# Optimization experiments

Measured on AMD Instinct MI355X. Metric: run time of the kernel, lower is better.

## Reference

```python
import jax, jax.numpy as jnp
import numpy as np

DIM = 2048
KV_DIM = 1024
NUM_HEADS = 16
HEAD_DIM = DIM // NUM_HEADS  # 128
EPS = 1e-6
B, LQ, LKV = 2, 4096, 1024


def _rope_cos_sin(L, d, base=10000.0):
    inv_freq = 1.0 / (base ** (np.arange(0, d, 2, dtype=np.float32) / d))  # [d/2]
    freqs = np.arange(L, dtype=np.float32)[:, None] * inv_freq[None, :]   # [L, d/2]
    emb = np.concatenate([freqs, freqs], axis=-1)                          # [L, d]
    return jnp.asarray(np.cos(emb)), jnp.asarray(np.sin(emb))


def setup_inputs() -> dict:
    key = jax.random.key(0)
    ks = jax.random.split(key, 10)
    x = jax.random.normal(ks[0], (B, LQ, DIM), dtype=jnp.float32)
    y = jax.random.normal(ks[1], (B, LKV, KV_DIM), dtype=jnp.float32)
    xc, xs = _rope_cos_sin(LQ, HEAD_DIM)
    yc, ys = _rope_cos_sin(LKV, HEAD_DIM)
    x_cos = jnp.broadcast_to(xc[None], (B, LQ, HEAD_DIM))
    x_sin = jnp.broadcast_to(xs[None], (B, LQ, HEAD_DIM))
    y_cos = jnp.broadcast_to(yc[None], (B, LKV, HEAD_DIM))
    y_sin = jnp.broadcast_to(ys[None], (B, LKV, HEAD_DIM))
    s = 0.02
    Wq = jax.random.normal(ks[2], (DIM, DIM), dtype=jnp.float32) * s
    Wk = jax.random.normal(ks[3], (DIM, KV_DIM), dtype=jnp.float32) * s
    Wv = jax.random.normal(ks[4], (DIM, KV_DIM), dtype=jnp.float32) * s
    Wo = jax.random.normal(ks[5], (DIM, DIM), dtype=jnp.float32) * s
    bq = jnp.zeros((DIM,), jnp.float32)
    bk = jnp.zeros((DIM,), jnp.float32)
    bv = jnp.zeros((DIM,), jnp.float32)
    bo = jnp.zeros((DIM,), jnp.float32)
    rmsq_w = jnp.ones((DIM,), jnp.float32)
    rmsk_w = jnp.ones((DIM,), jnp.float32)
    ln_w = jnp.ones((KV_DIM,), jnp.float32)
    ln_b = jnp.zeros((KV_DIM,), jnp.float32)
    return dict(x=x, y=y, x_cos=x_cos, x_sin=x_sin, y_cos=y_cos, y_sin=y_sin,
                Wq=Wq, bq=bq, Wk=Wk, bk=bk, Wv=Wv, bv=bv, Wo=Wo, bo=bo,
                rmsq_w=rmsq_w, rmsk_w=rmsk_w, ln_w=ln_w, ln_b=ln_b)


def _rms_norm(t, w, eps=EPS):
    return t * jax.lax.rsqrt(jnp.mean(t * t, axis=-1, keepdims=True) + eps) * w


def _layer_norm(t, w, b, eps=EPS):
    mu = jnp.mean(t, axis=-1, keepdims=True)
    var = jnp.mean(jnp.square(t - mu), axis=-1, keepdims=True)
    return (t - mu) * jax.lax.rsqrt(var + eps) * w + b


def _rotate_half(t):
    d2 = t.shape[-1] // 2
    return jnp.concatenate([-t[..., d2:], t[..., :d2]], axis=-1)


def _apply_rope(t, cos, sin):
    # t: [B, L, H, D]; cos/sin: [B, L, D] -> unsqueeze head dim (unsqueeze_dim=2)
    cos = cos[:, :, None, :]
    sin = sin[:, :, None, :]
    return t * cos + _rotate_half(t) * sin


def _block_forward(x, y, x_cos, x_sin, y_cos, y_sin,
                   Wq, bq, Wk, bk, Wv, bv, Wo, bo,
                   rmsq_w, rmsk_w, ln_w, ln_b):
    Bb, Lq, D = x.shape
    Lk = y.shape[1]
    H, Dh = NUM_HEADS, HEAD_DIM
    # y pre-norm (block-level LayerNorm)
    yn = _layer_norm(y, ln_w, ln_b)
    # projections + RMSNorm on q/k
    q = _rms_norm(x @ Wq.T + bq, rmsq_w)   # [B, Lq, D]
    k = _rms_norm(yn @ Wk.T + bk, rmsk_w)  # [B, Lk, D]
    v = yn @ Wv.T + bv                     # [B, Lk, D]
    # split heads and apply RoPE
    q = _apply_rope(q.reshape(Bb, Lq, H, Dh), x_cos, x_sin)
    k = _apply_rope(k.reshape(Bb, Lk, H, Dh), y_cos, y_sin)
    v = v.reshape(Bb, Lk, H, Dh)
    # non-causal cross attention, scale = 1/sqrt(head_dim)
    scale = 1.0 / jnp.sqrt(jnp.asarray(Dh, q.dtype))
    scores = jnp.einsum('blhd,bmhd->bhlm', q, k) * scale
    probs = jax.nn.softmax(scores, axis=-1)
    out = jnp.einsum('bhlm,bmhd->blhd', probs, v).reshape(Bb, Lq, D)
    return out @ Wo.T + bo


def reference(x, y, x_cos, x_sin, y_cos, y_sin,
              Wq, bq, Wk, bk, Wv, bv, Wo, bo,
              rmsq_w, rmsk_w, ln_w, ln_b):
    return _block_forward(x, y, x_cos, x_sin, y_cos, y_sin,
                          Wq, bq, Wk, bk, Wv, bv, Wo, bo,
                          rmsq_w, rmsk_w, ln_w, ln_b)
```

## Files before the change

### kernel.cpp

```cpp
#include <hip/hip_runtime.h>


typedef __attribute__((ext_vector_type(8))) short    short8;
typedef __attribute__((ext_vector_type(8))) unsigned short ushort8;
typedef __attribute__((ext_vector_type(4))) unsigned short ushort4v;
typedef __attribute__((ext_vector_type(4))) float    f32x4;
typedef __attribute__((ext_vector_type(16))) float   f32x16;
typedef __attribute__((ext_vector_type(4))) unsigned int uint4v;

#define DEV __device__ __forceinline__

DEV unsigned short f2bf(float f) {
  unsigned int u = __builtin_bit_cast(unsigned int, f);
  u += 0x7FFFu + ((u >> 16) & 1u);
  return (unsigned short)(u >> 16);
}
DEV float bf2f(unsigned short h) {
  return __builtin_bit_cast(float, ((unsigned int)h) << 16);
}
DEV unsigned int cvtpk_bf16(float lo, float hi) {
  unsigned int r;
  asm("v_cvt_pk_bf16_f32 %0, %1, %2" : "=v"(r) : "v"(lo), "v"(hi));
  return r;
}
DEV short8 mk8(unsigned a, unsigned b, unsigned c, unsigned d) {
  uint4v t; t.x = a; t.y = b; t.z = c; t.w = d;
  return __builtin_bit_cast(short8, t);
}

DEV void gload_lds16(const void* g, void* l) {
  __builtin_amdgcn_global_load_lds(
      (const __attribute__((address_space(1))) void*)g,
      (__attribute__((address_space(3))) void*)l, 16, 0, 0);
}

__global__ __launch_bounds__(256) void prep_kernel(const float* __restrict__ y,
                                                   const float* __restrict__ lnw,
                                                   const float* __restrict__ lnb,
                                                   unsigned short* __restrict__ yn,
                                                   const float* __restrict__ x,
                                                   const float* __restrict__ Wq,
                                                   const float* __restrict__ Wk,
                                                   const float* __restrict__ Wv,
                                                   const float* __restrict__ Wo,
                                                   unsigned short* __restrict__ xb,
                                                   unsigned short* __restrict__ Wqb,
                                                   unsigned short* __restrict__ Wkb,
                                                   unsigned short* __restrict__ Wvb,
                                                   unsigned short* __restrict__ Wob) {
  const int t = threadIdx.x;
  if (blockIdx.x < 2048) {
    const int row = blockIdx.x;
    const float* yr = y + (size_t)row * 1024;
    float4 v = *(const float4*)(yr + t * 4);
    float s1 = v.x + v.y + v.z + v.w;
    float s2 = v.x * v.x + v.y * v.y + v.z * v.z + v.w * v.w;
#pragma unroll
    for (int m = 1; m < 64; m <<= 1) {
      s1 += __shfl_xor(s1, m);
      s2 += __shfl_xor(s2, m);
    }
    __shared__ float red[8];
    const int wave = t >> 6, lane = t & 63;
    if (lane == 0) { red[wave] = s1; red[4 + wave] = s2; }
    __syncthreads();
    s1 = red[0] + red[1] + red[2] + red[3];
    s2 = red[4] + red[5] + red[6] + red[7];
    const float mu = s1 * (1.0f / 1024.0f);
    const float var = s2 * (1.0f / 1024.0f) - mu * mu;
    const float rs = rsqrtf(var + 1e-6f);
    ushort4v o;
    o.x = f2bf((v.x - mu) * rs * lnw[t * 4 + 0] + lnb[t * 4 + 0]);
    o.y = f2bf((v.y - mu) * rs * lnw[t * 4 + 1] + lnb[t * 4 + 1]);
    o.z = f2bf((v.z - mu) * rs * lnw[t * 4 + 2] + lnb[t * 4 + 2]);
    o.w = f2bf((v.w - mu) * rs * lnw[t * 4 + 3] + lnb[t * 4 + 3]);
    *(ushort4v*)(yn + (size_t)row * 1024 + t * 4) = o;
    return;
  }
  const int nx = 4194304, nwq = 1048576, nwk = 524288, nwv = 524288;
  const int total = 7340032;
  int i = (blockIdx.x - 2048) * 256 + t;
  const int stride = 1536 * 256;
  for (; i < total; i += stride) {
    int j = i;
    const float* s; unsigned short* d;
    if (j < nx) { s = x; d = xb; }
    else if ((j -= nx) < nwq) { s = Wq; d = Wqb; }
    else if ((j -= nwq) < nwk) { s = Wk; d = Wkb; }
    else if ((j -= nwk) < nwv) { s = Wv; d = Wvb; }
    else { j -= nwv; s = Wo; d = Wob; }
    float4 v = *(const float4*)(s + (size_t)j * 4);
    ushort4v o;
    o.x = f2bf(v.x); o.y = f2bf(v.y); o.z = f2bf(v.z); o.w = f2bf(v.w);
    *(ushort4v*)(d + (size_t)j * 4) = o;
  }
}

template <int EPI>
DEV void gemm256_body(const unsigned short* __restrict__ A,
                      const unsigned short* __restrict__ W,
                      const float* __restrict__ bias0,
                      const float* __restrict__ bias1,
                      int nsplit, void* __restrict__ Cout,
                      int M, int N, int K,
                      int bidLocal, int nwg, char* ldsb, int tid) {
  const int wave = tid >> 6, lane = tid & 63;
  const int lg = lane >> 4, l15 = lane & 15;
  const int wm = wave >> 2, wn = wave & 3;

  const int wgid = (bidLocal & 7) * (nwg >> 3) + (bidLocal >> 3);
  const int nbn = N >> 8;
  const int m0 = (wgid / nbn) * 256;
  const int n0 = (wgid % nbn) * 256;

  const char* Ab = (const char*)A;
  const char* Wb = (const char*)W;
  const size_t ld = (size_t)K * 2;
  const int NT = K >> 6;
  const int NI = NT >> 1;

  const int prow = tid >> 3;
  const int psw  = ((tid * 16) & 127) ^ ((prow & 7) << 4);
  const int pdst = tid * 16;
  const char* pAg = Ab + (size_t)(m0 + prow) * ld + psw;
  const char* pBg = Wb + (size_t)(n0 + prow) * ld + psw;

  f32x4 acc[8][4] = {};
  short8 af[4][2];
  short8 bf[4][2];

#define LDSB(BUF, SEG) (ldsb + ((BUF) * 4 + (SEG)) * 16384)

#define STG(BUF, HALF, ISB, TAU) do {                                         \
    const char* _g = ((ISB) ? pBg : pAg) + (size_t)(HALF) * 128 * ld +        \
                     (size_t)(TAU) * 128;                                     \
    char* _l = LDSB(BUF, (ISB) * 2 + (HALF));                                 \
    gload_lds16(_g, _l + pdst);                                               \
    gload_lds16(_g + 64 * ld, _l + pdst + 8192);                              \
  } while (0)

#define LDA(BUF, H) do {                                                      \
    const char* _b = LDSB(BUF, wm);                                           \
    _Pragma("unroll") for (int mfl = 0; mfl < 4; ++mfl) {                     \
      const int _r = (H) * 64 + mfl * 16 + l15;                               \
      _Pragma("unroll") for (int ks = 0; ks < 2; ++ks)                        \
        af[mfl][ks] = *(const short8*)(_b + _r * 128 +                        \
                        ((ks * 64 + lg * 16) ^ ((_r & 7) << 4)));             \
    }                                                                         \
  } while (0)

#define LDB(BUF, G) do {                                                      \
    const char* _b = LDSB(BUF, 2 + (wn >> 1));                                \
    _Pragma("unroll") for (int nfl = 0; nfl < 2; ++nfl) {                     \
      const int _r = (wn & 1) * 64 + (G) * 32 + nfl * 16 + l15;               \
      _Pragma("unroll") for (int ks = 0; ks < 2; ++ks)                        \
        bf[(G) * 2 + nfl][ks] = *(const short8*)(_b + _r * 128 +              \
                        ((ks * 64 + lg * 16) ^ ((_r & 7) << 4)));             \
    }                                                                         \
  } while (0)

#define MFMA_Q(H, G) do {                                                     \
    __builtin_amdgcn_s_setprio(1);                                            \
    _Pragma("unroll") for (int ks = 0; ks < 2; ++ks)                          \
    _Pragma("unroll") for (int mfl = 0; mfl < 4; ++mfl)                       \
    _Pragma("unroll") for (int nfl = 0; nfl < 2; ++nfl)                       \
      acc[(H) * 4 + mfl][(G) * 2 + nfl] =                                     \
        __builtin_amdgcn_mfma_f32_16x16x32_bf16(af[mfl][ks],                  \
            bf[(G) * 2 + nfl][ks], acc[(H) * 4 + mfl][(G) * 2 + nfl], 0,0,0); \
    __builtin_amdgcn_s_setprio(0);                                            \
  } while (0)

#define BAR() __builtin_amdgcn_s_barrier()
#define LGKM0() do { asm volatile("s_waitcnt lgkmcnt(0)" ::: "memory");       \
    __builtin_amdgcn_sched_barrier(0); } while (0)
#define VM4() asm volatile("s_waitcnt vmcnt(4)" ::: "memory")
#define VM0() asm volatile("s_waitcnt vmcnt(0)" ::: "memory")

  STG(0, 0, 0, 0); STG(0, 1, 0, 0); STG(0, 0, 1, 0); STG(0, 1, 1, 0);
  STG(1, 0, 1, 1); STG(1, 1, 1, 1);
  VM4(); BAR();

  for (int t = 0; t < NI - 1; ++t) {
    const int t2 = 2 * t;
    LDA(0, 0); LDB(0, 0); STG(1, 0, 0, t2 + 1);
    BAR(); LGKM0(); MFMA_Q(0, 0); BAR();
    LDB(0, 1); STG(1, 1, 0, t2 + 1);
    BAR(); LGKM0(); MFMA_Q(0, 1); BAR();
    LDA(0, 1); STG(0, 0, 1, t2 + 2);
    BAR(); LGKM0(); MFMA_Q(1, 1); BAR();
    STG(0, 1, 1, t2 + 2);
    BAR(); MFMA_Q(1, 0); VM4(); BAR();
    LDA(1, 0); LDB(1, 0); STG(0, 0, 0, t2 + 2);
    BAR(); LGKM0(); MFMA_Q(0, 0); BAR();
    LDB(1, 1); STG(0, 1, 0, t2 + 2);
    BAR(); LGKM0(); MFMA_Q(0, 1); BAR();
    LDA(1, 1); STG(1, 0, 1, t2 + 3);
    BAR(); LGKM0(); MFMA_Q(1, 1); BAR();
    STG(1, 1, 1, t2 + 3);
    BAR(); MFMA_Q(1, 0); VM4(); BAR();
  }

  LDA(0, 0); LDB(0, 0); STG(1, 0, 0, NT - 1);
  BAR(); LGKM0(); MFMA_Q(0, 0); BAR();
  LDB(0, 1); STG(1, 1, 0, NT - 1);
  BAR(); LGKM0(); MFMA_Q(0, 1); BAR();
  LDA(0, 1);
  BAR(); LGKM0(); MFMA_Q(1, 1); BAR();
  BAR(); MFMA_Q(1, 0); VM0(); BAR();
  LDA(1, 0); LDB(1, 0); LGKM0(); MFMA_Q(0, 0);
  LDB(1, 1); LGKM0(); MFMA_Q(0, 1);
  LDA(1, 1); LGKM0(); MFMA_Q(1, 1);
  MFMA_Q(1, 0);

#undef STG
#undef LDA
#undef LDB
#undef MFMA_Q
#undef BAR
#undef LGKM0
#undef VM4
#undef VM0
#undef LDSB

#pragma unroll
  for (int nf = 0; nf < 4; ++nf) {
    const int n = n0 + wn * 64 + nf * 16 + l15;
    const float bv = (n < nsplit) ? bias0[n] : bias1[n - nsplit];
#pragma unroll
    for (int mf = 0; mf < 8; ++mf) {
      const int mB = m0 + wm * 128 + mf * 16 + lg * 4;
#pragma unroll
      for (int r = 0; r < 4; ++r) {
        const float v = acc[mf][nf][r] + bv;
        if constexpr (EPI == 0)
          ((unsigned short*)Cout)[(size_t)(mB + r) * N + n] = f2bf(v);
        else
          ((float*)Cout)[(size_t)(mB + r) * N + n] = v;
      }
    }
  }
}

__global__ __launch_bounds__(512, 2) void gemm_dual(const unsigned short* __restrict__ xb,
                                                    const unsigned short* __restrict__ Wqb,
                                                    const float* __restrict__ bq,
                                                    unsigned short* __restrict__ qpre,
                                                    const unsigned short* __restrict__ ynb,
                                                    const unsigned short* __restrict__ Wkb,
                                                    const float* __restrict__ bk,
                                                    const float* __restrict__ bv,
                                                    unsigned short* __restrict__ kvpre) {
  __shared__ __align__(16) char lds[2][4][16384];
  if (blockIdx.x < 256)
    gemm256_body<0>(xb, Wqb, bq, bq, 2048, qpre, 8192, 2048, 2048,
                    blockIdx.x, 256, &lds[0][0][0], threadIdx.x);
  else
    gemm256_body<0>(ynb, Wkb, bk, bv, 2048, kvpre, 2048, 4096, 1024,
                    blockIdx.x - 256, 128, &lds[0][0][0], threadIdx.x);
}

__global__ __launch_bounds__(512, 2) void gemm_f32(const unsigned short* __restrict__ A,
                                                   const unsigned short* __restrict__ W,
                                                   const float* __restrict__ bias,
                                                   float* __restrict__ C,
                                                   int M, int N, int K) {
  __shared__ __align__(16) char lds[2][4][16384];
  gemm256_body<1>(A, W, bias, bias, N, C, M, N, K,
                  blockIdx.x, 256, &lds[0][0][0], threadIdx.x);
}

DEV void rmsrope_body(const unsigned short* __restrict__ in,
                      const float* __restrict__ w,
                      const float* __restrict__ cs,
                      const float* __restrict__ sn,
                      unsigned short* __restrict__ out,
                      int L, int ldin, float scale, int row,
                      unsigned short* srow, float* red) {
  const int t = threadIdx.x;
  const unsigned short* ir = in + (size_t)row * ldin;
  ushort8 v = *(const ushort8*)(ir + t * 8);
  float vals[8];
  float ss = 0.f;
#pragma unroll
  for (int j = 0; j < 8; ++j) { vals[j] = bf2f(v[j]); ss += vals[j] * vals[j]; }
  *(ushort8*)(srow + t * 8) = v;
#pragma unroll
  for (int m = 1; m < 64; m <<= 1) ss += __shfl_xor(ss, m);
  const int wave = t >> 6, lane = t & 63;
  if (lane == 0) red[wave] = ss;
  __syncthreads();
  const float tot = red[0] + red[1] + red[2] + red[3];
  const float rms = rsqrtf(tot * (1.0f / 2048.0f) + 1e-6f);

  const int n0 = t * 8;
  const int d0 = n0 & 127;
  const int hh = n0 >> 7;
  const float sign = (d0 < 64) ? -1.0f : 1.0f;
  const float* cb = cs + (size_t)row * 128 + d0;
  const float* sb = sn + (size_t)row * 128 + d0;
  ushort8 po = *(const ushort8*)(srow + (n0 ^ 64));
  ushort8 ou;
#pragma unroll
  for (int j = 0; j < 8; ++j) {
    const float self = vals[j] * rms * w[n0 + j];
    const float part = bf2f(po[j]) * rms * w[(n0 ^ 64) + j];
    ou[j] = f2bf((self * cb[j] + sign * part * sb[j]) * scale);
  }
  const int b = row / L, l = row - (row / L) * L;
  *(ushort8*)(out + (((size_t)(b * 16 + hh)) * L + l) * 128 + d0) = ou;
}

DEV void vtrans_body(const unsigned short* __restrict__ vpre,
                     unsigned short* __restrict__ vt, int ldv, int bid,
                     unsigned short (*lt)[130]) {
  const int kt = bid & 15, bh = bid >> 4;
  const int h = bh & 15, b = bh >> 4;
  const int t = threadIdx.x;
  const int i0 = t >> 4, c0 = (t & 15) * 8;
  const unsigned short* src = vpre + ((size_t)(b * 1024 + kt * 64)) * ldv + h * 128;
#pragma unroll
  for (int ii = 0; ii < 4; ++ii) {
    const int i = i0 + ii * 16;
    ushort8 v = *(const ushort8*)(src + (size_t)i * ldv + c0);
#pragma unroll
    for (int j = 0; j < 8; ++j) lt[i][c0 + j] = v[j];
  }
  __syncthreads();
  const int d0 = t >> 3, j0 = (t & 7) * 8;
  unsigned short* dst = vt + (size_t)bh * 128 * 1024 + kt * 64;
#pragma unroll
  for (int dd = 0; dd < 4; ++dd) {
    const int d = d0 + dd * 32;
    ushort8 o;
#pragma unroll
    for (int jj = 0; jj < 8; ++jj) o[jj] = lt[j0 + jj][d];
    *(ushort8*)(dst + (size_t)d * 1024 + j0) = o;
  }
}

__global__ __launch_bounds__(256) void post_kernel(const unsigned short* __restrict__ qpre,
                                                   const float* __restrict__ rmsq_w,
                                                   const float* __restrict__ x_cos,
                                                   const float* __restrict__ x_sin,
                                                   unsigned short* __restrict__ qr,
                                                   const unsigned short* __restrict__ kvpre,
                                                   const float* __restrict__ rmsk_w,
                                                   const float* __restrict__ y_cos,
                                                   const float* __restrict__ y_sin,
                                                   unsigned short* __restrict__ kr,
                                                   unsigned short* __restrict__ vt,
                                                   float qscale) {
  __shared__ __align__(16) unsigned short srow[2048];
  __shared__ float red[4];
  __shared__ unsigned short lt[64][130];
  const int b = blockIdx.x;
  if (b < 8192) {
    rmsrope_body(qpre, rmsq_w, x_cos, x_sin, qr, 4096, 2048, qscale, b, srow, red);
  } else if (b < 10240) {
    rmsrope_body(kvpre, rmsk_w, y_cos, y_sin, kr, 1024, 4096, 1.0f, b - 8192, srow, red);
  } else {
    vtrans_body(kvpre + 2048, vt, 4096, b - 10240, lt);
  }
}

__global__ __launch_bounds__(512, 2) void attn_kernel(const unsigned short* __restrict__ q,
                                                      const unsigned short* __restrict__ k,
                                                      const unsigned short* __restrict__ vt,
                                                      unsigned short* __restrict__ ao) {
  __shared__ __align__(16) char sK[2][2][64 * 256];
  __shared__ __align__(16) char sV[2][2][64 * 256];

  const int bid0 = blockIdx.x;
  const int bid = (bid0 & 7) * 64 + (bid0 >> 3);
  const int qt = bid & 15, bh = bid >> 4;
  const int tid = threadIdx.x;
  const int wave = tid >> 6, lane = tid & 63;
  const int l31 = lane & 31, hi = lane >> 5;
  const bool hib = (hi != 0);

  const unsigned short* qbase = q + (((size_t)bh * 4096) + qt * 256 + wave * 32) * 128;
  const char* kbase = (const char*)(k + (size_t)bh * 1024 * 128);
  const char* vbase = (const char*)(vt + (size_t)bh * 128 * 1024);

  short8 qb[8];
#pragma unroll
  for (int step = 0; step < 8; ++step)
    qb[step] = *(const short8*)(qbase + (size_t)l31 * 128 + step * 16 + hi * 8);

  f32x16 o[4] = {};
  float lsum = 0.f;

#define STAGE_KV(BUF, KV0) do {                                              \
    _Pragma("unroll")                                                        \
    for (int sub = 0; sub < 2; ++sub) {                                      \
      _Pragma("unroll")                                                      \
      for (int i = 0; i < 2; ++i) {                                          \
        const int p = (i * 512 + tid) * 16;                                  \
        const int row = p >> 8;                                              \
        const int si = (p & 255) ^ ((row & 15) << 4);                        \
        gload_lds16(kbase + (size_t)((KV0) + sub * 64 + row) * 256 + si,     \
                    sK[BUF][sub] + p);                                       \
      }                                                                      \
      _Pragma("unroll")                                                      \
      for (int i = 0; i < 2; ++i) {                                          \
        const int p = (i * 512 + tid) * 16;                                  \
        const int row = p >> 8;                                              \
        const int si = (p & 255) ^ ((row & 15) << 4);                        \
        const int d = 2 * row + (si >> 7);                                   \
        gload_lds16(vbase + (size_t)d * 2048 + ((KV0) + sub * 64) * 2 +      \
                    (si & 127), sV[BUF][sub] + p);                           \
      }                                                                      \
    }                                                                        \
  } while (0)

#define QK(K, S0, S1) do {                                                   \
    const int ksw = (l31 & 15) << 4;                                         \
    _Pragma("unroll") for (int step = 0; step < 8; ++step) {                 \
      const int cb2 = step * 32 + hi * 16;                                   \
      short8 kf0 = *(const short8*)((K) + l31 * 256 + (cb2 ^ ksw));          \
      short8 kf1 = *(const short8*)((K) + (32 + l31) * 256 + (cb2 ^ ksw));   \
      S0 = __builtin_amdgcn_mfma_f32_32x32x16_bf16(kf0, qb[step], S0, 0,0,0);\
      S1 = __builtin_amdgcn_mfma_f32_32x32x16_bf16(kf1, qb[step], S1, 0,0,0);\
    }                                                                        \
  } while (0)

#define SOFTMAX_PV(V, SS, F) do {                                            \
    float p_[16];                                                            \
    _Pragma("unroll") for (int r = 0; r < 16; ++r) p_[r] = exp2f((SS)[r]);   \
    lsum += (((p_[0]+p_[1])+(p_[2]+p_[3])) + ((p_[4]+p_[5])+(p_[6]+p_[7])))  \
          + (((p_[8]+p_[9])+(p_[10]+p_[11])) + ((p_[12]+p_[13])+(p_[14]+p_[15])));\
    const unsigned w0 = cvtpk_bf16(p_[0], p_[1]),  w1 = cvtpk_bf16(p_[2], p_[3]), \
                   w2 = cvtpk_bf16(p_[4], p_[5]),  w3 = cvtpk_bf16(p_[6], p_[7]), \
                   w4 = cvtpk_bf16(p_[8], p_[9]),  w5 = cvtpk_bf16(p_[10], p_[11]),\
                   w6 = cvtpk_bf16(p_[12], p_[13]),w7 = cvtpk_bf16(p_[14], p_[15]);\
    const unsigned x0 = (unsigned)__shfl_xor((int)(hib ? w0 : w2), 32);      \
    const unsigned x1 = (unsigned)__shfl_xor((int)(hib ? w1 : w3), 32);      \
    const unsigned x2 = (unsigned)__shfl_xor((int)(hib ? w4 : w6), 32);      \
    const unsigned x3 = (unsigned)__shfl_xor((int)(hib ? w5 : w7), 32);      \
    const short8 fr0 = mk8(hib ? x0 : w0, hib ? x1 : w1,                     \
                           hib ? w2 : x0, hib ? w3 : x1);                    \
    const short8 fr1 = mk8(hib ? x2 : w4, hib ? x3 : w5,                     \
                           hib ? w6 : x2, hib ? w7 : x3);                    \
    _Pragma("unroll") for (int kstep = 0; kstep < 2; ++kstep) {              \
      const short8 pa = kstep ? fr1 : fr0;                                   \
      const int colb = (F) * 64 + kstep * 32 + hi * 16;                      \
      _Pragma("unroll") for (int dt = 0; dt < 4; ++dt) {                     \
        const int vrow = dt * 16 + (l31 >> 1);                               \
        const int inner = (l31 & 1) * 128 + colb;                            \
        short8 vf = *(const short8*)((V) + vrow * 256 +                      \
                                     (inner ^ ((vrow & 15) << 4)));          \
        o[dt] = __builtin_amdgcn_mfma_f32_32x32x16_bf16(pa, vf, o[dt], 0,0,0);\
      }                                                                      \
    }                                                                        \
  } while (0)

#define TILE(BUF) do {                                                       \
    f32x16 s0 = {}, s1 = {}, s2 = {}, s3 = {};                               \
    QK(sK[BUF][0], s0, s1);                                                  \
    QK(sK[BUF][1], s2, s3);                                                  \
    SOFTMAX_PV(sV[BUF][0], s0, 0);                                           \
    SOFTMAX_PV(sV[BUF][0], s1, 1);                                           \
    SOFTMAX_PV(sV[BUF][1], s2, 0);                                           \
    SOFTMAX_PV(sV[BUF][1], s3, 1);                                           \
  } while (0)

  STAGE_KV(0, 0);
  __syncthreads();

#pragma unroll 1
  for (int kt2 = 0; kt2 < 4; ++kt2) {
    STAGE_KV(1, (2 * kt2 + 1) * 128);
    TILE(0);
    __syncthreads();
    if (kt2 < 3) STAGE_KV(0, (2 * kt2 + 2) * 128);
    TILE(1);
    __syncthreads();
  }
#undef STAGE_KV
#undef QK
#undef SOFTMAX_PV
#undef TILE

  lsum += __shfl_xor(lsum, 32);
  const float linv = 1.0f / lsum;
  const int b = bh >> 4, h = bh & 15;
#pragma unroll
  for (int r = 0; r < 16; ++r) {
    const int crow = (r & 3) + 8 * (r >> 2) + 4 * hi;
    const float inv = __shfl(linv, crow);
    const int qg = qt * 256 + wave * 32 + crow;
    const size_t orow = ((size_t)b * 4096 + qg) * 2048 + h * 128;
#pragma unroll
    for (int dt = 0; dt < 4; ++dt)
      ao[orow + dt * 32 + l31] = f2bf(o[dt][r] * inv);
  }
}

extern "C" void kernel_launch(void* const* d_in, const int* in_sizes, int n_in,
                              void* d_out, int out_size, void* d_ws, size_t ws_size,
                              hipStream_t stream) {
  (void)in_sizes; (void)n_in; (void)out_size; (void)ws_size;
  const float* x      = (const float*)d_in[0];
  const float* y      = (const float*)d_in[1];
  const float* x_cos  = (const float*)d_in[2];
  const float* x_sin  = (const float*)d_in[3];
  const float* y_cos  = (const float*)d_in[4];
  const float* y_sin  = (const float*)d_in[5];
  const float* Wq     = (const float*)d_in[6];
  const float* bq     = (const float*)d_in[7];
  const float* Wk     = (const float*)d_in[8];
  const float* bk     = (const float*)d_in[9];
  const float* Wv     = (const float*)d_in[10];
  const float* bv     = (const float*)d_in[11];
  const float* Wo     = (const float*)d_in[12];
  const float* bo     = (const float*)d_in[13];
  const float* rmsq_w = (const float*)d_in[14];
  const float* rmsk_w = (const float*)d_in[15];
  const float* ln_w   = (const float*)d_in[16];
  const float* ln_b   = (const float*)d_in[17];

  char* ws = (char*)d_ws;
  unsigned short* xb    = (unsigned short*)(ws + 0);
  unsigned short* Wqb   = (unsigned short*)(ws + 33554432);
  unsigned short* Wkb   = (unsigned short*)(ws + 41943040);
  unsigned short* Wvb   = (unsigned short*)(ws + 46137344);
  unsigned short* Wob   = (unsigned short*)(ws + 50331648);
  unsigned short* ynb   = (unsigned short*)(ws + 58720256);
  unsigned short* qpre  = (unsigned short*)(ws + 62914560);
  unsigned short* kvpre = (unsigned short*)(ws + 96468992);
  unsigned short* qr    = (unsigned short*)(ws + 113246208);
  unsigned short* kr    = (unsigned short*)(ws + 33554432);
  unsigned short* vt    = (unsigned short*)(ws + 41943040);
  unsigned short* ao    = xb;
  (void)Wvb;

  const float qscale = 1.4426950408889634f * 0.08838834764831843f;

  prep_kernel<<<3584, 256, 0, stream>>>(y, ln_w, ln_b, ynb, x, Wq, Wk, Wv, Wo,
                                        xb, Wqb, Wkb, Wvb, Wob);
  gemm_dual<<<384, 512, 0, stream>>>(xb, Wqb, bq, qpre, ynb, Wkb, bk, bv, kvpre);
  post_kernel<<<10752, 256, 0, stream>>>(qpre, rmsq_w, x_cos, x_sin, qr,
                                         kvpre, rmsk_w, y_cos, y_sin, kr, vt, qscale);
  attn_kernel<<<512, 512, 0, stream>>>(qr, kr, vt, ao);
  gemm_f32<<<256, 512, 0, stream>>>(ao, Wob, bo, (float*)d_out, 8192, 2048, 2048);
}
```

Before: 303.4 us.

## Split KV projection over K across all GEMM blocks and reduce in post kernel

```diff
diff --git a/kernel.cpp b/kernel.cpp
--- a/kernel.cpp
+++ b/kernel.cpp
@@ -102,7 +102,7 @@
                       const float* __restrict__ bias0,
                       const float* __restrict__ bias1,
                       int nsplit, void* __restrict__ Cout,
-                      int M, int N, int K,
+                      int M, int N, int K, int ldRow,
                       int bidLocal, int nwg, char* ldsb, int tid) {
   const int wave = tid >> 6, lane = tid & 63;
   const int lg = lane >> 4, l15 = lane & 15;
@@ -115,7 +115,7 @@
 
   const char* Ab = (const char*)A;
   const char* Wb = (const char*)W;
-  const size_t ld = (size_t)K * 2;
+  const size_t ld = (size_t)ldRow * 2;
   const int NT = K >> 6;
   const int NI = NT >> 1;
 
@@ -225,17 +225,18 @@
 #pragma unroll
   for (int nf = 0; nf < 4; ++nf) {
     const int n = n0 + wn * 64 + nf * 16 + l15;
-    const float bv = (n < nsplit) ? bias0[n] : bias1[n - nsplit];
+    float bv = 0.f;
+    if constexpr (EPI != 2) bv = (n < nsplit) ? bias0[n] : bias1[n - nsplit];
 #pragma unroll
     for (int mf = 0; mf < 8; ++mf) {
       const int mB = m0 + wm * 128 + mf * 16 + lg * 4;
 #pragma unroll
       for (int r = 0; r < 4; ++r) {
         const float v = acc[mf][nf][r] + bv;
-        if constexpr (EPI == 0)
+        if constexpr (EPI == 1)
+          ((float*)Cout)[(size_t)(mB + r) * N + n] = v;
+        else
           ((unsigned short*)Cout)[(size_t)(mB + r) * N + n] = f2bf(v);
-        else
-          ((float*)Cout)[(size_t)(mB + r) * N + n] = v;
       }
     }
   }
@@ -247,16 +248,16 @@
                                                     unsigned short* __restrict__ qpre,
                                                     const unsigned short* __restrict__ ynb,
                                                     const unsigned short* __restrict__ Wkb,
-                                                    const float* __restrict__ bk,
-                                                    const float* __restrict__ bv,
-                                                    unsigned short* __restrict__ kvpre) {
+                                                    unsigned short* __restrict__ kvpA,
+                                                    unsigned short* __restrict__ kvpB) {
   __shared__ __align__(16) char lds[2][4][16384];
-  if (blockIdx.x < 256)
-    gemm256_body<0>(xb, Wqb, bq, bq, 2048, qpre, 8192, 2048, 2048,
-                    blockIdx.x, 256, &lds[0][0][0], threadIdx.x);
-  else
-    gemm256_body<0>(ynb, Wkb, bk, bv, 2048, kvpre, 2048, 4096, 1024,
-                    blockIdx.x - 256, 128, &lds[0][0][0], threadIdx.x);
+  gemm256_body<0>(xb, Wqb, bq, bq, 2048, qpre, 8192, 2048, 2048, 2048,
+                  blockIdx.x, 256, &lds[0][0][0], threadIdx.x);
+  __syncthreads();
+  const int kvt = blockIdx.x & 127, khalf = blockIdx.x >> 7;
+  gemm256_body<2>(ynb + khalf * 512, Wkb + khalf * 512, nullptr, nullptr, 0,
+                  khalf ? kvpB : kvpA, 2048, 4096, 512, 1024,
+                  kvt, 128, &lds[0][0][0], threadIdx.x);
 }
 
 __global__ __launch_bounds__(512, 2) void gemm_f32(const unsigned short* __restrict__ A,
@@ -265,25 +266,33 @@
                                                    float* __restrict__ C,
                                                    int M, int N, int K) {
   __shared__ __align__(16) char lds[2][4][16384];
-  gemm256_body<1>(A, W, bias, bias, N, C, M, N, K,
+  gemm256_body<1>(A, W, bias, bias, N, C, M, N, K, K,
                   blockIdx.x, 256, &lds[0][0][0], threadIdx.x);
 }
 
-DEV void rmsrope_body(const unsigned short* __restrict__ in,
-                      const float* __restrict__ w,
-                      const float* __restrict__ cs,
-                      const float* __restrict__ sn,
-                      unsigned short* __restrict__ out,
-                      int L, int ldin, float scale, int row,
-                      unsigned short* srow, float* red) {
+DEV void rmsrope2_body(const unsigned short* __restrict__ in,
+                       const unsigned short* __restrict__ in2,
+                       const float* __restrict__ bias,
+                       const float* __restrict__ w,
+                       const float* __restrict__ cs,
+                       const float* __restrict__ sn,
+                       unsigned short* __restrict__ out,
+                       int L, int ldin, float scale, int row,
+                       float* srow, float* red) {
   const int t = threadIdx.x;
-  const unsigned short* ir = in + (size_t)row * ldin;
-  ushort8 v = *(const ushort8*)(ir + t * 8);
+  ushort8 v = *(const ushort8*)(in + (size_t)row * ldin + t * 8);
   float vals[8];
+  if (in2) {
+    ushort8 v2 = *(const ushort8*)(in2 + (size_t)row * ldin + t * 8);
+#pragma unroll
+    for (int j = 0; j < 8; ++j) vals[j] = bf2f(v[j]) + bf2f(v2[j]) + bias[t * 8 + j];
+  } else {
+#pragma unroll
+    for (int j = 0; j < 8; ++j) vals[j] = bf2f(v[j]);
+  }
   float ss = 0.f;
 #pragma unroll
-  for (int j = 0; j < 8; ++j) { vals[j] = bf2f(v[j]); ss += vals[j] * vals[j]; }
-  *(ushort8*)(srow + t * 8) = v;
+  for (int j = 0; j < 8; ++j) { ss += vals[j] * vals[j]; srow[t * 8 + j] = vals[j]; }
 #pragma unroll
   for (int m = 1; m < 64; m <<= 1) ss += __shfl_xor(ss, m);
   const int wave = t >> 6, lane = t & 63;
@@ -298,32 +307,35 @@
   const float sign = (d0 < 64) ? -1.0f : 1.0f;
   const float* cb = cs + (size_t)row * 128 + d0;
   const float* sb = sn + (size_t)row * 128 + d0;
-  ushort8 po = *(const ushort8*)(srow + (n0 ^ 64));
   ushort8 ou;
 #pragma unroll
   for (int j = 0; j < 8; ++j) {
     const float self = vals[j] * rms * w[n0 + j];
-    const float part = bf2f(po[j]) * rms * w[(n0 ^ 64) + j];
+    const float part = srow[(n0 ^ 64) + j] * rms * w[(n0 ^ 64) + j];
     ou[j] = f2bf((self * cb[j] + sign * part * sb[j]) * scale);
   }
   const int b = row / L, l = row - (row / L) * L;
   *(ushort8*)(out + (((size_t)(b * 16 + hh)) * L + l) * 128 + d0) = ou;
 }
 
-DEV void vtrans_body(const unsigned short* __restrict__ vpre,
-                     unsigned short* __restrict__ vt, int ldv, int bid,
-                     unsigned short (*lt)[130]) {
+DEV void vtrans2_body(const unsigned short* __restrict__ va,
+                      const unsigned short* __restrict__ vb,
+                      const float* __restrict__ bv,
+                      unsigned short* __restrict__ vt, int ldv, int bid,
+                      unsigned short (*lt)[130]) {
   const int kt = bid & 15, bh = bid >> 4;
   const int h = bh & 15, b = bh >> 4;
   const int t = threadIdx.x;
   const int i0 = t >> 4, c0 = (t & 15) * 8;
-  const unsigned short* src = vpre + ((size_t)(b * 1024 + kt * 64)) * ldv + h * 128;
+  const size_t sbase = ((size_t)(b * 1024 + kt * 64)) * ldv + h * 128;
 #pragma unroll
   for (int ii = 0; ii < 4; ++ii) {
     const int i = i0 + ii * 16;
-    ushort8 v = *(const ushort8*)(src + (size_t)i * ldv + c0);
-#pragma unroll
-    for (int j = 0; j < 8; ++j) lt[i][c0 + j] = v[j];
+    ushort8 a = *(const ushort8*)(va + sbase + (size_t)i * ldv + c0);
+    ushort8 bb = *(const ushort8*)(vb + sbase + (size_t)i * ldv + c0);
+#pragma unroll
+    for (int j = 0; j < 8; ++j)
+      lt[i][c0 + j] = f2bf(bf2f(a[j]) + bf2f(bb[j]) + bv[h * 128 + c0 + j]);
   }
   __syncthreads();
   const int d0 = t >> 3, j0 = (t & 7) * 8;
@@ -343,23 +355,28 @@
                                                    const float* __restrict__ x_cos,
                                                    const float* __restrict__ x_sin,
                                                    unsigned short* __restrict__ qr,
-                                                   const unsigned short* __restrict__ kvpre,
+                                                   const unsigned short* __restrict__ kvpA,
+                                                   const unsigned short* __restrict__ kvpB,
+                                                   const float* __restrict__ bk,
+                                                   const float* __restrict__ bv,
                                                    const float* __restrict__ rmsk_w,
                                                    const float* __restrict__ y_cos,
                                                    const float* __restrict__ y_sin,
                                                    unsigned short* __restrict__ kr,
                                                    unsigned short* __restrict__ vt,
                                                    float qscale) {
-  __shared__ __align__(16) unsigned short srow[2048];
+  __shared__ __align__(16) float srow[2048];
   __shared__ float red[4];
   __shared__ unsigned short lt[64][130];
   const int b = blockIdx.x;
   if (b < 8192) {
-    rmsrope_body(qpre, rmsq_w, x_cos, x_sin, qr, 4096, 2048, qscale, b, srow, red);
+    rmsrope2_body(qpre, nullptr, nullptr, rmsq_w, x_cos, x_sin, qr,
+                  4096, 2048, qscale, b, srow, red);
   } else if (b < 10240) {
-    rmsrope_body(kvpre, rmsk_w, y_cos, y_sin, kr, 1024, 4096, 1.0f, b - 8192, srow, red);
+    rmsrope2_body(kvpA, kvpB, bk, rmsk_w, y_cos, y_sin, kr,
+                  1024, 4096, 1.0f, b - 8192, srow, red);
   } else {
-    vtrans_body(kvpre + 2048, vt, 4096, b - 10240, lt);
+    vtrans2_body(kvpA + 2048, kvpB + 2048, bv, vt, 4096, b - 10240, lt);
   }
 }
 
@@ -527,20 +544,22 @@
   unsigned short* Wob   = (unsigned short*)(ws + 50331648);
   unsigned short* ynb   = (unsigned short*)(ws + 58720256);
   unsigned short* qpre  = (unsigned short*)(ws + 62914560);
-  unsigned short* kvpre = (unsigned short*)(ws + 96468992);
-  unsigned short* qr    = (unsigned short*)(ws + 113246208);
-  unsigned short* kr    = (unsigned short*)(ws + 33554432);
-  unsigned short* vt    = (unsigned short*)(ws + 41943040);
-  unsigned short* ao    = xb;
+  unsigned short* kvpA  = (unsigned short*)(ws + 96468992);
+  unsigned short* kvpB  = (unsigned short*)(ws + 113246208);
+  unsigned short* qr    = xb;
+  unsigned short* kr    = Wqb;
+  unsigned short* vt    = Wkb;
+  unsigned short* ao    = qpre;
   (void)Wvb;
 
   const float qscale = 1.4426950408889634f * 0.08838834764831843f;
 
   prep_kernel<<<3584, 256, 0, stream>>>(y, ln_w, ln_b, ynb, x, Wq, Wk, Wv, Wo,
                                         xb, Wqb, Wkb, Wvb, Wob);
-  gemm_dual<<<384, 512, 0, stream>>>(xb, Wqb, bq, qpre, ynb, Wkb, bk, bv, kvpre);
+  gemm_dual<<<256, 512, 0, stream>>>(xb, Wqb, bq, qpre, ynb, Wkb, kvpA, kvpB);
   post_kernel<<<10752, 256, 0, stream>>>(qpre, rmsq_w, x_cos, x_sin, qr,
-                                         kvpre, rmsk_w, y_cos, y_sin, kr, vt, qscale);
+                                         kvpA, kvpB, bk, bv, rmsk_w,
+                                         y_cos, y_sin, kr, vt, qscale);
   attn_kernel<<<512, 512, 0, stream>>>(qr, kr, vt, ao);
   gemm_f32<<<256, 512, 0, stream>>>(ao, Wob, bo, (float*)d_out, 8192, 2048, 2048);
 }
```

Result: no change. 303.3 us (-0.0%).
